# Optimization experiments

Measured on AMD Instinct MI355X. Metric: run time of the kernel, lower is better.

Reference implementation:

```python
import jax, jax.numpy as jnp
import numpy as np

B, H, L, E, M = 16, 8, 4096, 64, 64


def setup_inputs() -> dict:
    key = jax.random.key(0)
    k1, k2, k3 = jax.random.split(key, 3)
    x = jax.random.normal(k1, (B, H, L, E), dtype=jnp.float32)
    # nn.Parameter(torch.randn(E, E, M, 2) / sqrt(E))
    weights = jax.random.normal(k2, (E, E, M, 2), dtype=jnp.float32) / np.float32(np.sqrt(E))
    # torch.randperm(L//2)[:M].sort()[0] -> sorted unique mode indices in [0, L//2)
    index = jnp.sort(jax.random.permutation(k3, L // 2)[:M]).astype(jnp.int32)
    return {"x": x, "weights": weights, "index": index}


def reference(x, weights, index):
    Bx, Hx, Lx, Ex = x.shape
    xt = jnp.swapaxes(x, -1, -2)                      # [B,H,E,L]
    x_ft = jnp.fft.rfft(xt, axis=-1)                  # [B,H,E,L//2+1] complex64
    w_c = jax.lax.complex(weights[..., 0], weights[..., 1])  # [E,E,M] complex
    sel = x_ft[..., index]                            # gather K modes: [B,H,E,M]
    out_sel = jnp.einsum('bhei,eoi->bhoi', sel, w_c)  # per-mode complex matmul
    out_ft = jnp.zeros_like(x_ft).at[..., index].set(out_sel)  # scatter back
    out = jnp.fft.irfft(out_ft, n=Lx, axis=-1)        # [B,H,E,L] real
    return jnp.swapaxes(out, -1, -2)                  # [B,H,L,E]
```

## Files before the change

### kernel.cpp

```cpp
#include <hip/hip_runtime.h>

using half8 = __attribute__((ext_vector_type(8))) _Float16;
using f32x4 = __attribute__((ext_vector_type(4))) float;

#define Lc 4096
#define Ec 64
#define Mc 64
#define BHc 128

#define TWO_PI_OVER_L 1.5339807878856412e-3f

__global__ __launch_bounds__(256) void twid_k(const int* __restrict__ idx,
                                              _Float16* __restrict__ Tt,
                                              _Float16* __restrict__ UL) {
    int id = blockIdx.x * 256 + threadIdx.x;
    {
        int l = id >> 7, m2 = id & 127, m = m2 & 63;
        int k = idx[m];
        int ph = (k * l) & (Lc - 1);
        float s, c;
        sincosf((float)ph * TWO_PI_OVER_L, &s, &c);
        UL[id] = (_Float16)((m2 >= 64) ? s : c);
    }
    {
        int m2 = id >> 12, l = id & 4095, m = m2 & 63;
        int k = idx[m];
        int ph = (k * l) & (Lc - 1);
        float s, c;
        sincosf((float)ph * TWO_PI_OVER_L, &s, &c);
        Tt[id] = (_Float16)((m2 >= 64) ? -s : c);
    }
}

template<int NCH>
__global__ __launch_bounds__(256) void fwd_k(const float* __restrict__ x,
                                             const _Float16* __restrict__ Tt,
                                             float* __restrict__ selP) {
    constexpr int CH = Lc / NCH;
    constexpr int NT = CH / 64;
    __shared__ _Float16 xs[64 * 64];
    int bh = blockIdx.x, ch = blockIdx.y;
    int tid = threadIdx.x;
    int lane = tid & 63, w = tid >> 6;
    int lo16 = lane & 15, kg = lane >> 4;
    int col4 = tid & 15, lp = tid >> 4;

    const float* xp = x + ((size_t)bh * Lc + (size_t)ch * CH) * Ec + col4 * 4;
    const _Float16* tp = Tt + (size_t)(w * 32 + lo16) * Lc + ch * CH + kg * 8;

    float4 xa[2], xb[2];
    #pragma unroll
    for (int i = 0; i < 2; ++i) {
        const float* g = xp + (size_t)(2 * lp + 32 * i) * Ec;
        xa[i] = *(const float4*)g;
        xb[i] = *(const float4*)(g + Ec);
    }

    f32x4 acc[2][4] = {};
    for (int s = 0; s < NT; ++s) {
        unsigned int pk[2][4];
        #pragma unroll
        for (int i = 0; i < 2; ++i) {
            const float* pa = (const float*)&xa[i];
            const float* pb = (const float*)&xb[i];
            #pragma unroll
            for (int j = 0; j < 4; ++j) {
                unsigned short ua = __builtin_bit_cast(unsigned short, (_Float16)pa[j]);
                unsigned short ub = __builtin_bit_cast(unsigned short, (_Float16)pb[j]);
                pk[i][j] = ua | ((unsigned int)ub << 16);
            }
        }
        __syncthreads();
        #pragma unroll
        for (int i = 0; i < 2; ++i)
            #pragma unroll
            for (int j = 0; j < 4; ++j) {
                int jr = (j + col4) & 3;
                int e = col4 * 4 + jr;
                int byt = (e * 128 + lp * 4 + i * 64) ^ ((e & 7) << 4);
                *(unsigned int*)((char*)xs + byt) = pk[i][jr];
            }
        __syncthreads();
        if (s + 1 < NT) {
            #pragma unroll
            for (int i = 0; i < 2; ++i) {
                const float* g = xp + (size_t)((s + 1) * 64 + 2 * lp + 32 * i) * Ec;
                xa[i] = *(const float4*)g;
                xb[i] = *(const float4*)(g + Ec);
            }
        }
        #pragma unroll
        for (int ks = 0; ks < 2; ++ks) {
            half8 A0 = *(const half8*)(tp + s * 64 + ks * 32);
            half8 A1 = *(const half8*)(tp + (size_t)16 * Lc + s * 64 + ks * 32);
            #pragma unroll
            for (int j = 0; j < 4; ++j) {
                int rb = ((16 * j + lo16) * 128 + ks * 64 + kg * 16) ^ ((lo16 & 7) << 4);
                half8 B = *(const half8*)((const char*)xs + rb);
                acc[0][j] = __builtin_amdgcn_mfma_f32_16x16x32_f16(A0, B, acc[0][j], 0, 0, 0);
                acc[1][j] = __builtin_amdgcn_mfma_f32_16x16x32_f16(A1, B, acc[1][j], 0, 0, 0);
            }
        }
    }
    float* op = selP + (size_t)(ch * BHc + bh) * (128 * Ec);
    #pragma unroll
    for (int a = 0; a < 2; ++a)
        #pragma unroll
        for (int j = 0; j < 4; ++j)
            #pragma unroll
            for (int r = 0; r < 4; ++r) {
                int m2 = w * 32 + a * 16 + kg * 4 + r;
                int e  = 16 * j + lo16;
                op[m2 * Ec + e] = acc[a][j][r];
            }
}

__global__ __launch_bounds__(256) void mix_k(const float* __restrict__ selP,
                                             const float* __restrict__ wgt,
                                             const int* __restrict__ idx,
                                             _Float16* __restrict__ Vt, int nch) {
    __shared__ float sel_s[128 * 65];
    int bh = blockIdx.x, oh = blockIdx.y;
    int tid = threadIdx.x;
    #pragma unroll
    for (int i = 0; i < 8; ++i) {
        int f4 = i * 256 + tid;
        float4 a = make_float4(0.f, 0.f, 0.f, 0.f);
        for (int chn = 0; chn < nch; ++chn) {
            float4 v = *((const float4*)(selP + (size_t)(chn * BHc + bh) * 8192) + f4);
            a.x += v.x; a.y += v.y; a.z += v.z; a.w += v.w;
        }
        int m2 = f4 >> 4, e4 = (f4 & 15) * 4;
        float* dst = &sel_s[m2 * 65 + e4];
        dst[0] = a.x; dst[1] = a.y; dst[2] = a.z; dst[3] = a.w;
    }
    __syncthreads();
    int og = tid & 7, mg = tid >> 3;
    int o0 = oh * 32 + og * 4;
    int m0 = mg * 2;
    float rR[4][2] = {{0}}, rI[4][2] = {{0}};
    for (int e = 0; e < Ec; ++e) {
        float sr0 = sel_s[m0 * 65 + e];
        float sr1 = sel_s[(m0 + 1) * 65 + e];
        float si0 = sel_s[(64 + m0) * 65 + e];
        float si1 = sel_s[(64 + m0 + 1) * 65 + e];
        #pragma unroll
        for (int i = 0; i < 4; ++i) {
            const float4* wp = (const float4*)&wgt[(((size_t)e * Ec + (o0 + i)) * Mc + m0) * 2];
            float4 wv = *wp;
            rR[i][0] += sr0 * wv.x - si0 * wv.y;
            rI[i][0] += sr0 * wv.y + si0 * wv.x;
            rR[i][1] += sr1 * wv.z - si1 * wv.w;
            rI[i][1] += sr1 * wv.w + si1 * wv.z;
        }
    }
    float s0 = (idx[m0] == 0 ? 1.0f : 2.0f) / (float)Lc;
    float s1 = (idx[m0 + 1] == 0 ? 1.0f : 2.0f) / (float)Lc;
    #pragma unroll
    for (int i = 0; i < 4; ++i) {
        _Float16* vp = Vt + ((size_t)bh * 64 + o0 + i) * 128;
        unsigned short r0 = __builtin_bit_cast(unsigned short, (_Float16)(rR[i][0] * s0));
        unsigned short r1 = __builtin_bit_cast(unsigned short, (_Float16)(rR[i][1] * s1));
        unsigned short i0 = __builtin_bit_cast(unsigned short, (_Float16)(-rI[i][0] * s0));
        unsigned short i1 = __builtin_bit_cast(unsigned short, (_Float16)(-rI[i][1] * s1));
        *(unsigned int*)&vp[m0]      = r0 | ((unsigned int)r1 << 16);
        *(unsigned int*)&vp[64 + m0] = i0 | ((unsigned int)i1 << 16);
    }
}

__global__ __launch_bounds__(256) void inv_k(const _Float16* __restrict__ UL,
                                             const _Float16* __restrict__ Vt,
                                             float* __restrict__ out) {
    __shared__ _Float16 vs[64 * 136];
    int bh = blockIdx.x, lb = blockIdx.y;
    int tid = threadIdx.x, lane = tid & 63, w = tid >> 6;
    int lo16 = lane & 15, kg = lane >> 4;
    #pragma unroll
    for (int i = 0; i < 4; ++i) {
        int f = i * 256 + tid;
        int row = f >> 4, seg = f & 15;
        uint4 t4 = *(const uint4*)(Vt + (size_t)bh * 8192 + row * 128 + seg * 8);
        *(uint4*)&vs[row * 136 + seg * 8] = t4;
    }
    __syncthreads();
    int lt0 = lb * 256 + w * 64;
    const _Float16* up = UL + (size_t)(lt0 + lo16) * 128 + kg * 8;
    f32x4 acc[4][4] = {};
    #pragma unroll
    for (int ks = 0; ks < 4; ++ks) {
        half8 Af[4];
        #pragma unroll
        for (int a = 0; a < 4; ++a)
            Af[a] = *(const half8*)(up + (size_t)a * 16 * 128 + ks * 32);
        #pragma unroll
        for (int j = 0; j < 4; ++j) {
            half8 Bf = *(const half8*)&vs[(16 * j + lo16) * 136 + ks * 32 + kg * 8];
            #pragma unroll
            for (int a = 0; a < 4; ++a)
                acc[a][j] = __builtin_amdgcn_mfma_f32_16x16x32_f16(Af[a], Bf, acc[a][j], 0, 0, 0);
        }
    }
    float* op = out + ((size_t)bh * Lc + lt0) * Ec;
    #pragma unroll
    for (int a = 0; a < 4; ++a)
        #pragma unroll
        for (int j = 0; j < 4; ++j)
            #pragma unroll
            for (int r = 0; r < 4; ++r) {
                int ll = a * 16 + kg * 4 + r;
                int o  = 16 * j + lo16;
                op[ll * Ec + o] = acc[a][j][r];
            }
}

extern "C" void kernel_launch(void* const* d_in, const int* in_sizes, int n_in,
                              void* d_out, int out_size, void* d_ws, size_t ws_size,
                              hipStream_t stream) {
    const float* x   = (const float*)d_in[0];
    const float* wgt = (const float*)d_in[1];
    const int*   idx = (const int*)d_in[2];
    float* out = (float*)d_out;

    size_t need8 = (size_t)8 * BHc * 8192 * 4 + (2ull * 128 * Lc + (size_t)BHc * 8192) * 2;
    int nch = (ws_size >= need8) ? 8 : 4;

    char* ws = (char*)d_ws;
    float*    selP = (float*)ws;
    _Float16* Tt   = (_Float16*)(ws + (size_t)nch * BHc * 8192 * 4);
    _Float16* UL   = Tt + (size_t)128 * Lc;
    _Float16* Vt   = UL + (size_t)Lc * 128;

    twid_k<<<2048, 256, 0, stream>>>(idx, Tt, UL);
    if (nch == 8)
        fwd_k<8><<<dim3(BHc, 8), 256, 0, stream>>>(x, Tt, selP);
    else
        fwd_k<4><<<dim3(BHc, 4), 256, 0, stream>>>(x, Tt, selP);
    mix_k<<<dim3(BHc, 2), 256, 0, stream>>>(selP, wgt, idx, Vt, nch);
    inv_k<<<dim3(BHc, 16), 256, 0, stream>>>(UL, Vt, out);
}
```

Measured before the change: 129.8 us.

## Drop LDS staging in forward and inverse kernels, load fragments from global

The forward DFT kernel no longer converts x tiles to fp16 through swizzled shared memory with barriers. Each wave now loads its own 16-column slice of x straight from global as strided scalar loads, builds the B fragment in registers, and loops over all 8 mode tiles. The inverse kernel likewise reads Vt fragments directly from global instead of copying them to LDS first. This removes the barriers and LDS traffic, at the cost of uncoalesced scalar 4-byte global loads with an 256-byte stride in the forward kernel, and redundant global reads of the twiddle table across waves.

```diff
diff --git a/kernel.cpp b/kernel.cpp
--- a/kernel.cpp
+++ b/kernel.cpp
@@ -37,82 +37,38 @@
                                              const _Float16* __restrict__ Tt,
                                              float* __restrict__ selP) {
     constexpr int CH = Lc / NCH;
-    constexpr int NT = CH / 64;
-    __shared__ _Float16 xs[64 * 64];
+    constexpr int NS = CH / 32;
     int bh = blockIdx.x, ch = blockIdx.y;
-    int tid = threadIdx.x;
-    int lane = tid & 63, w = tid >> 6;
+    int tid = threadIdx.x, lane = tid & 63, w = tid >> 6;
     int lo16 = lane & 15, kg = lane >> 4;
-    int col4 = tid & 15, lp = tid >> 4;
 
-    const float* xp = x + ((size_t)bh * Lc + (size_t)ch * CH) * Ec + col4 * 4;
-    const _Float16* tp = Tt + (size_t)(w * 32 + lo16) * Lc + ch * CH + kg * 8;
+    const float* xp = x + ((size_t)bh * Lc + (size_t)ch * CH + kg * 8) * Ec
+                        + w * 16 + lo16;
+    const _Float16* tp = Tt + (size_t)lo16 * Lc + ch * CH + kg * 8;
 
-    float4 xa[2], xb[2];
-    #pragma unroll
-    for (int i = 0; i < 2; ++i) {
-        const float* g = xp + (size_t)(2 * lp + 32 * i) * Ec;
-        xa[i] = *(const float4*)g;
-        xb[i] = *(const float4*)(g + Ec);
-    }
-
-    f32x4 acc[2][4] = {};
-    for (int s = 0; s < NT; ++s) {
-        unsigned int pk[2][4];
+    f32x4 acc[8] = {};
+    for (int s = 0; s < NS; ++s) {
+        const float* gx = xp + (size_t)s * 32 * Ec;
+        float f[8];
         #pragma unroll
-        for (int i = 0; i < 2; ++i) {
-            const float* pa = (const float*)&xa[i];
-            const float* pb = (const float*)&xb[i];
-            #pragma unroll
-            for (int j = 0; j < 4; ++j) {
-                unsigned short ua = __builtin_bit_cast(unsigned short, (_Float16)pa[j]);
-                unsigned short ub = __builtin_bit_cast(unsigned short, (_Float16)pb[j]);
-                pk[i][j] = ua | ((unsigned int)ub << 16);
-            }
-        }
-        __syncthreads();
+        for (int i = 0; i < 8; ++i) f[i] = gx[(size_t)i * Ec];
+        half8 B;
         #pragma unroll
-        for (int i = 0; i < 2; ++i)
-            #pragma unroll
-            for (int j = 0; j < 4; ++j) {
-                int jr = (j + col4) & 3;
-                int e = col4 * 4 + jr;
-                int byt = (e * 128 + lp * 4 + i * 64) ^ ((e & 7) << 4);
-                *(unsigned int*)((char*)xs + byt) = pk[i][jr];
-            }
-        __syncthreads();
-        if (s + 1 < NT) {
-            #pragma unroll
-            for (int i = 0; i < 2; ++i) {
-                const float* g = xp + (size_t)((s + 1) * 64 + 2 * lp + 32 * i) * Ec;
-                xa[i] = *(const float4*)g;
-                xb[i] = *(const float4*)(g + Ec);
-            }
-        }
+        for (int i = 0; i < 8; ++i) B[i] = (_Float16)f[i];
         #pragma unroll
-        for (int ks = 0; ks < 2; ++ks) {
-            half8 A0 = *(const half8*)(tp + s * 64 + ks * 32);
-            half8 A1 = *(const half8*)(tp + (size_t)16 * Lc + s * 64 + ks * 32);
-            #pragma unroll
-            for (int j = 0; j < 4; ++j) {
-                int rb = ((16 * j + lo16) * 128 + ks * 64 + kg * 16) ^ ((lo16 & 7) << 4);
-                half8 B = *(const half8*)((const char*)xs + rb);
-                acc[0][j] = __builtin_amdgcn_mfma_f32_16x16x32_f16(A0, B, acc[0][j], 0, 0, 0);
-                acc[1][j] = __builtin_amdgcn_mfma_f32_16x16x32_f16(A1, B, acc[1][j], 0, 0, 0);
-            }
+        for (int a = 0; a < 8; ++a) {
+            half8 A = *(const half8*)(tp + (size_t)a * 16 * Lc + s * 32);
+            acc[a] = __builtin_amdgcn_mfma_f32_16x16x32_f16(A, B, acc[a], 0, 0, 0);
         }
     }
     float* op = selP + (size_t)(ch * BHc + bh) * (128 * Ec);
     #pragma unroll
-    for (int a = 0; a < 2; ++a)
+    for (int a = 0; a < 8; ++a)
         #pragma unroll
-        for (int j = 0; j < 4; ++j)
-            #pragma unroll
-            for (int r = 0; r < 4; ++r) {
-                int m2 = w * 32 + a * 16 + kg * 4 + r;
-                int e  = 16 * j + lo16;
-                op[m2 * Ec + e] = acc[a][j][r];
-            }
+        for (int r = 0; r < 4; ++r) {
+            int m2 = a * 16 + kg * 4 + r;
+            op[m2 * Ec + w * 16 + lo16] = acc[a][r];
+        }
 }
 
 __global__ __launch_bounds__(256) void mix_k(const float* __restrict__ selP,
@@ -171,34 +127,27 @@
 __global__ __launch_bounds__(256) void inv_k(const _Float16* __restrict__ UL,
                                              const _Float16* __restrict__ Vt,
                                              float* __restrict__ out) {
-    __shared__ _Float16 vs[64 * 136];
     int bh = blockIdx.x, lb = blockIdx.y;
     int tid = threadIdx.x, lane = tid & 63, w = tid >> 6;
     int lo16 = lane & 15, kg = lane >> 4;
-    #pragma unroll
-    for (int i = 0; i < 4; ++i) {
-        int f = i * 256 + tid;
-        int row = f >> 4, seg = f & 15;
-        uint4 t4 = *(const uint4*)(Vt + (size_t)bh * 8192 + row * 128 + seg * 8);
-        *(uint4*)&vs[row * 136 + seg * 8] = t4;
-    }
-    __syncthreads();
     int lt0 = lb * 256 + w * 64;
     const _Float16* up = UL + (size_t)(lt0 + lo16) * 128 + kg * 8;
+    const _Float16* vp = Vt + (size_t)bh * 8192 + (size_t)lo16 * 128 + kg * 8;
     f32x4 acc[4][4] = {};
     #pragma unroll
     for (int ks = 0; ks < 4; ++ks) {
-        half8 Af[4];
+        half8 Af[4], Bf[4];
         #pragma unroll
         for (int a = 0; a < 4; ++a)
             Af[a] = *(const half8*)(up + (size_t)a * 16 * 128 + ks * 32);
         #pragma unroll
-        for (int j = 0; j < 4; ++j) {
-            half8 Bf = *(const half8*)&vs[(16 * j + lo16) * 136 + ks * 32 + kg * 8];
+        for (int j = 0; j < 4; ++j)
+            Bf[j] = *(const half8*)(vp + (size_t)j * 16 * 128 + ks * 32);
+        #pragma unroll
+        for (int j = 0; j < 4; ++j)
             #pragma unroll
             for (int a = 0; a < 4; ++a)
-                acc[a][j] = __builtin_amdgcn_mfma_f32_16x16x32_f16(Af[a], Bf, acc[a][j], 0, 0, 0);
-        }
+                acc[a][j] = __builtin_amdgcn_mfma_f32_16x16x32_f16(Af[a], Bf[j], acc[a][j], 0, 0, 0);
     }
     float* op = out + ((size_t)bh * Lc + lt0) * Ec;
     #pragma unroll
```

After: 176.1 us. 35.7% more time.
